# Performance work log

Measured on AMD Instinct MI355X. Metric: run time of the kernel, lower is better.

## Reference

```python
import jax, jax.numpy as jnp
import numpy as np
import math

D_MODEL = 1024
N_HEADS = 8
HEAD_DIM = D_MODEL // N_HEADS
N_CLASSES = 2


def setup_inputs() -> dict:
    key = jax.random.key(0)
    ks = jax.random.split(key, 12)
    s = 1.0 / math.sqrt(D_MODEL)
    return {
        "x": jax.random.normal(ks[0], (8192, D_MODEL), dtype=jnp.float32),
        "class_token": jax.random.normal(ks[1], (1, 1, D_MODEL), dtype=jnp.float32),
        "Wq": jax.random.normal(ks[2], (D_MODEL, D_MODEL), dtype=jnp.float32) * s,
        "bq": jnp.zeros((D_MODEL,), jnp.float32),
        "Wk": jax.random.normal(ks[3], (D_MODEL, D_MODEL), dtype=jnp.float32) * s,
        "bk": jnp.zeros((D_MODEL,), jnp.float32),
        "Wv": jax.random.normal(ks[4], (D_MODEL, D_MODEL), dtype=jnp.float32) * s,
        "bv": jnp.zeros((D_MODEL,), jnp.float32),
        "Wo": jax.random.normal(ks[5], (D_MODEL, D_MODEL), dtype=jnp.float32) * s,
        "bo": jnp.zeros((D_MODEL,), jnp.float32),
        "Wc": jax.random.normal(ks[6], (N_CLASSES, D_MODEL), dtype=jnp.float32) * s,
        "bc": jnp.zeros((N_CLASSES,), jnp.float32),
    }


def reference(x, class_token, Wq, bq, Wk, bk, Wv, bv, Wo, bo, Wc, bc):
    # Prepend class token: [T, D] with T = N_patches + 1 (batch size is 1)
    tokens = jnp.concatenate([class_token.reshape(1, D_MODEL), x], axis=0)
    T = tokens.shape[0]
    scale = 1.0 / math.sqrt(HEAD_DIM)

    def heads(W, b):
        return (tokens @ W.T + b).reshape(T, N_HEADS, HEAD_DIM).transpose(1, 0, 2)

    q = heads(Wq, bq)  # [H, T, hd]
    k = heads(Wk, bk)
    v = heads(Wv, bv)

    scores = jnp.einsum("htd,hsd->hts", q, k) * scale  # [H, T, T]
    probs = jax.nn.softmax(scores, axis=-1)
    attn_out = jnp.einsum("hts,hsd->htd", probs, v)  # [H, T, hd]

    # MIL attention weights: class-token row, over patches, head-averaged
    A = probs[:, 0, 1:].mean(axis=0)[None, :]  # [1, N_patches]

    out = attn_out.transpose(1, 0, 2).reshape(T, D_MODEL) @ Wo.T + bo  # [T, D]
    cls_out = out[0:1]  # [1, D]

    logits = cls_out @ Wc.T + bc  # [1, n_classes]
    y_probs = jax.nn.softmax(logits, axis=1)

    m = jnp.argmax(y_probs.reshape(-1))
    row = m // N_CLASSES
    Y_hat = (m % N_CLASSES)[None]  # [1]
    top_instance = jnp.take(logits, row, axis=0)[None]  # [1, n_classes]
    Y_prob = jnp.take(y_probs, row, axis=0)[None]  # [1, n_classes]

    return top_instance, Y_prob, Y_hat, y_probs, A
```

## Files before the change

kernel.cpp:

```cpp
#include <hip/hip_runtime.h>
#include <math.h>

#define D 1024
#define NH 8
#define T 8193

#define OFF_QCLS  0
#define OFF_EP    1024
#define OFF_W     17408
#define OFF_G     25600
#define OFF_CH    41984
#define OFF_CONST 41992
#define OFF_L     42000
#define OFF_PLOG  44048
#define OFF_SCT   48144

static __device__ __forceinline__ float wred(float v) {
    #pragma unroll
    for (int m = 32; m; m >>= 1) v += __shfl_xor(v, m, 64);
    return v;
}

#define DPPADD(v, ctrl) \
    ((v) + __int_as_float(__builtin_amdgcn_update_dpp( \
        0, __float_as_int(v), (ctrl), 0xf, 0xf, true)))

static __device__ __forceinline__ float wave_total(float v) {
    v = DPPADD(v, 0x111);
    v = DPPADD(v, 0x112);
    v = DPPADD(v, 0x114);
    v = DPPADD(v, 0x118);
    v = DPPADD(v, 0x142);
    v = DPPADD(v, 0x143);
    return __int_as_float(__builtin_amdgcn_readlane(__float_as_int(v), 63));
}

__global__ __launch_bounds__(1024) void k1(const float* __restrict__ Wq,
                                           const float* __restrict__ bq,
                                           const float* __restrict__ ct,
                                           const float* __restrict__ Wc,
                                           const float* __restrict__ Wo,
                                           float* __restrict__ ws) {
    __shared__ float red[16];
    __shared__ float er[4][2][256];
    const int b = blockIdx.x, t = threadIdx.x;
    const int w = t >> 6, lane = t & 63;
    if (b < 256) {
        int grp = t >> 8, f4 = t & 255;
        int r = b * 4 + grp;
        const float4* wr = (const float4*)(Wq + (size_t)r * D);
        const float4* cv = (const float4*)ct;
        float4 a = wr[f4], c = cv[f4];
        float v = a.x*c.x + a.y*c.y + a.z*c.z + a.w*c.w;
        v = wred(v);
        if (lane == 0) red[w] = v;
        __syncthreads();
        if (t < 4)
            ws[OFF_QCLS + b*4 + t] = red[4*t]+red[4*t+1]+red[4*t+2]+red[4*t+3] + bq[b*4 + t];
    } else {
        int idx = b - 256;
        int p = idx >> 2, jq = idx & 3;
        int layer = t >> 8, jl = t & 255;
        int j = jq * 256 + jl;
        int i0 = p * 128 + layer * 32;
        const float* wo = Wo + (size_t)i0 * D + j;
        float a0 = 0.f, a1 = 0.f;
        #pragma unroll 8
        for (int i = 0; i < 32; ++i) {
            float r = wo[(size_t)i * D];
            a0 += Wc[i0 + i] * r;
            a1 += Wc[D + i0 + i] * r;
        }
        er[layer][0][jl] = a0;
        er[layer][1][jl] = a1;
        __syncthreads();
        if (t < 512) {
            int c = t >> 8, jl2 = t & 255;
            ws[OFF_EP + p*2048 + c*1024 + jq*256 + jl2] =
                er[0][c][jl2] + er[1][c][jl2] + er[2][c][jl2] + er[3][c][jl2];
        }
    }
}

__global__ __launch_bounds__(1024) void k2(const float* __restrict__ Wk,
                                           const float* __restrict__ bk,
                                           const float* __restrict__ Wv,
                                           const float* __restrict__ Wc,
                                           const float* __restrict__ bo,
                                           const float* __restrict__ bv,
                                           const float* __restrict__ bc,
                                           float* __restrict__ ws) {
    __shared__ float qh[128];
    __shared__ float el[2][128];
    __shared__ float lw[8][128];
    __shared__ float lg[8][2][128];
    __shared__ float red[32];
    const int b = blockIdx.x, t = threadIdx.x;
    const int w = t >> 6, lane = t & 63;
    if (b < 64) {
        int h = b >> 3, je = b & 7;
        if (t < 128) qh[t] = ws[OFF_QCLS + h*128 + t];
        __syncthreads();
        int layer = t >> 7, jl = t & 127;
        int j = je * 128 + jl, d0 = layer * 16;
        const float* wk = Wk + (size_t)(h*128 + d0) * D + j;
        float acc = 0.f;
        #pragma unroll 8
        for (int d = 0; d < 16; ++d) acc += qh[d0 + d] * wk[(size_t)d * D];
        lw[layer][jl] = acc;
        __syncthreads();
        if (t < 128) {
            float s = 0.f;
            #pragma unroll
            for (int i = 0; i < 8; ++i) s += lw[i][t];
            ws[OFF_W + h*1024 + je*128 + t] = s;
        }
    } else if (b < 128) {
        int hb = b - 64, h = hb >> 3, je = hb & 7;
        if (t < 256) {
            int c = t >> 7, r = t & 127;
            float s = 0.f;
            #pragma unroll
            for (int p = 0; p < 8; ++p) s += ws[OFF_EP + p*2048 + c*1024 + h*128 + r];
            el[c][r] = s;
        }
        __syncthreads();
        int layer = t >> 7, jl = t & 127;
        int j = je * 128 + jl, r0 = layer * 16;
        const float* wv = Wv + (size_t)(h*128 + r0) * D + j;
        float a0 = 0.f, a1 = 0.f;
        #pragma unroll 8
        for (int r = 0; r < 16; ++r) {
            float xv = wv[(size_t)r * D];
            a0 += el[0][r0 + r] * xv;
            a1 += el[1][r0 + r] * xv;
        }
        lg[layer][0][jl] = a0;
        lg[layer][1][jl] = a1;
        __syncthreads();
        if (t < 256) {
            int c = t >> 7, jl2 = t & 127;
            float s = 0.f;
            #pragma unroll
            for (int i = 0; i < 8; ++i) s += lg[i][c][jl2];
            ws[OFF_G + c*8192 + h*1024 + je*128 + jl2] = s;
        }
    } else if (b == 128) {
        int h = t >> 7, d = t & 127;
        float v = ws[OFF_QCLS + h*128 + d] * bk[h*128 + d];
        v = wred(v);
        if (lane == 0) red[w] = v;
        __syncthreads();
        if (t < 8) ws[OFF_CH + t] = red[2*t] + red[2*t+1];
    } else {
        float e0 = 0.f, e1 = 0.f;
        #pragma unroll
        for (int p = 0; p < 8; ++p) {
            e0 += ws[OFF_EP + p*2048 + t];
            e1 += ws[OFF_EP + p*2048 + 1024 + t];
        }
        float v0 = Wc[t]*bo[t] + e0*bv[t];
        float v1 = Wc[D + t]*bo[t] + e1*bv[t];
        v0 = wred(v0); v1 = wred(v1);
        if (lane == 0) { red[w] = v0; red[16 + w] = v1; }
        __syncthreads();
        if (t == 0) {
            float a0 = 0.f, a1 = 0.f;
            #pragma unroll
            for (int i = 0; i < 16; ++i) { a0 += red[i]; a1 += red[16 + i]; }
            ws[OFF_CONST + 0] = a0 + bc[0];
            ws[OFF_CONST + 1] = a1 + bc[1];
        }
    }
}

__global__ __launch_bounds__(512, 2) void k3(const float* __restrict__ x,
                                             const float* __restrict__ ct,
                                             float* __restrict__ ws) {
    __shared__ float stash[33 * D];
    __shared__ float pe[33][8];
    __shared__ float plred[8][8];
    const int b = blockIdx.x, t = threadIdx.x;
    const int w = t >> 6, lane = t & 63;

    float4 wreg[8][4];
    const float4* wg4 = (const float4*)(ws + OFF_W);
    #pragma unroll
    for (int h = 0; h < 8; ++h)
        #pragma unroll
        for (int j = 0; j < 4; ++j)
            wreg[h][j] = wg4[h * 256 + j * 64 + lane];
    float chv[8];
    #pragma unroll
    for (int h = 0; h < 8; ++h) chv[h] = ws[OFF_CH + h];

    const int ntok_blk = (b == 255) ? 33 : 32;
    const bool tail = (b == 255 && w == 7);
    const int ntok_w = tail ? 5 : 4;
    for (int i = 0; i < ntok_w; ++i) {
        int k = (i < 4) ? (w * 4 + i) : 32;
        int s = b * 32 + k;
        const float* row = (s == 0) ? ct : (x + (size_t)(s - 1) * D);
        float* dst = stash + k * D;
        #pragma unroll
        for (int q = 0; q < 4; ++q)
            __builtin_amdgcn_global_load_lds(
                (const __attribute__((address_space(1))) unsigned int*)(row + q * 256 + lane * 4),
                (__attribute__((address_space(3))) unsigned int*)(dst + q * 256),
                16, 0, 0);
    }

    const float scale = 0.08838834764831845f;
    auto compute = [&](int k) {
        int s = b * 32 + k;
        const float4* tk = (const float4*)(stash + k * D);
        float4 t0 = tk[lane], t1 = tk[64 + lane], t2 = tk[128 + lane], t3 = tk[192 + lane];
        float pv[8];
        #pragma unroll
        for (int h = 0; h < 8; ++h) {
            float4 w0 = wreg[h][0], w1 = wreg[h][1], w2 = wreg[h][2], w3 = wreg[h][3];
            float v = w0.x*t0.x + w0.y*t0.y + w0.z*t0.z + w0.w*t0.w
                    + w1.x*t1.x + w1.y*t1.y + w1.z*t1.z + w1.w*t1.w
                    + w2.x*t2.x + w2.y*t2.y + w2.z*t2.z + w2.w*t2.w
                    + w3.x*t3.x + w3.y*t3.y + w3.z*t3.z + w3.w*t3.w;
            v = wave_total(v);
            pv[h] = __expf(scale * (v + chv[h]));
        }
        if (lane == 0) {
            float4* sct = (float4*)(ws + OFF_SCT);
            sct[s * 2]     = make_float4(pv[0], pv[1], pv[2], pv[3]);
            sct[s * 2 + 1] = make_float4(pv[4], pv[5], pv[6], pv[7]);
            *(float4*)&pe[k][0] = make_float4(pv[0], pv[1], pv[2], pv[3]);
            *(float4*)&pe[k][4] = make_float4(pv[4], pv[5], pv[6], pv[7]);
        }
    };

    if (!tail) {
        __builtin_amdgcn_s_waitcnt(0x0f7c); compute(w*4 + 0);
        __builtin_amdgcn_s_waitcnt(0x0f78); compute(w*4 + 1);
        __builtin_amdgcn_s_waitcnt(0x0f74); compute(w*4 + 2);
        __builtin_amdgcn_s_waitcnt(0x0f70); compute(w*4 + 3);
    } else {
        __builtin_amdgcn_s_waitcnt(0x0f70);
        for (int i = 0; i < 5; ++i) compute((i < 4) ? (w*4 + i) : 32);
    }
    __syncthreads();

    if (t < 8) {
        float s = 0.f;
        for (int k = 0; k < ntok_blk; ++k) s += pe[k][t];
        ws[OFF_L + b * 8 + t] = s;
    }

    const int f4 = t & 255, half = t >> 8;
    const float4* st4 = (const float4*)stash;
    float4 acc0 = {0,0,0,0}, acc1 = {0,0,0,0}, acc2 = {0,0,0,0}, acc3 = {0,0,0,0};
    for (int k = 0; k < ntok_blk; ++k) {
        float4 tv = st4[k * 256 + f4];
        float4 pv = *(const float4*)&pe[k][half * 4];
        acc0.x += pv.x*tv.x; acc0.y += pv.x*tv.y; acc0.z += pv.x*tv.z; acc0.w += pv.x*tv.w;
        acc1.x += pv.y*tv.x; acc1.y += pv.y*tv.y; acc1.z += pv.y*tv.z; acc1.w += pv.y*tv.w;
        acc2.x += pv.z*tv.x; acc2.y += pv.z*tv.y; acc2.z += pv.z*tv.z; acc2.w += pv.z*tv.w;
        acc3.x += pv.w*tv.x; acc3.y += pv.w*tv.y; acc3.z += pv.w*tv.z; acc3.w += pv.w*tv.w;
    }

    const float4* G4 = (const float4*)(ws + OFF_G);
    float pl[8];
    #pragma unroll
    for (int c = 0; c < 2; ++c) {
        float4 g0 = G4[c*2048 + (half*4 + 0)*256 + f4];
        float4 g1 = G4[c*2048 + (half*4 + 1)*256 + f4];
        float4 g2 = G4[c*2048 + (half*4 + 2)*256 + f4];
        float4 g3 = G4[c*2048 + (half*4 + 3)*256 + f4];
        pl[c*4+0] = g0.x*acc0.x + g0.y*acc0.y + g0.z*acc0.z + g0.w*acc0.w;
        pl[c*4+1] = g1.x*acc1.x + g1.y*acc1.y + g1.z*acc1.z + g1.w*acc1.w;
        pl[c*4+2] = g2.x*acc2.x + g2.y*acc2.y + g2.z*acc2.z + g2.w*acc2.w;
        pl[c*4+3] = g3.x*acc3.x + g3.y*acc3.y + g3.z*acc3.z + g3.w*acc3.w;
    }
    #pragma unroll
    for (int v = 0; v < 8; ++v) pl[v] = wave_total(pl[v]);
    if (lane == 0)
        #pragma unroll
        for (int v = 0; v < 8; ++v) plred[w][v] = pl[v];
    __syncthreads();
    if (t < 16) {
        int c = t >> 3, hh = t & 7;
        int wb = (hh < 4) ? 0 : 4, vi = c * 4 + (hh & 3);
        ws[OFF_PLOG + b*16 + t] =
            plred[wb][vi] + plred[wb+1][vi] + plred[wb+2][vi] + plred[wb+3][vi];
    }
}

__global__ __launch_bounds__(256) void k4(float* __restrict__ out,
                                          float* __restrict__ ws) {
    __shared__ float lp[32][8];
    __shared__ float rlh[8];
    __shared__ float r2[8];
    const int b = blockIdx.x, t = threadIdx.x;

    {
        int seg = t >> 3, h = t & 7;
        float s = 0.f;
        for (int pb = seg; pb < 256; pb += 32) s += ws[OFF_L + pb*8 + h];
        lp[seg][h] = s;
    }
    __syncthreads();
    if (t < 8) {
        float s = 0.f;
        #pragma unroll
        for (int i = 0; i < 32; ++i) s += lp[i][t];
        rlh[t] = 1.f / s;
    }
    __syncthreads();

    if (t < 32) {
        int s_ = b * 32 + t + 1;
        const float4* sct = (const float4*)(ws + OFF_SCT);
        float4 pa = sct[s_ * 2], pb4 = sct[s_ * 2 + 1];
        float sum = pa.x*rlh[0] + pa.y*rlh[1] + pa.z*rlh[2] + pa.w*rlh[3]
                  + pb4.x*rlh[4] + pb4.y*rlh[5] + pb4.z*rlh[6] + pb4.w*rlh[7];
        out[6 + s_] = sum * 0.125f;
    }

    if (b == 0) {
        float v0 = 0.f, v1 = 0.f;
        for (int idx = t; idx < 4096; idx += 256) {
            float val = ws[OFF_PLOG + idx];
            int rem = idx & 15;
            float z = val * rlh[rem & 7];
            if ((rem >> 3) == 0) v0 += z; else v1 += z;
        }
        v0 = wred(v0); v1 = wred(v1);
        if ((t & 63) == 0) { r2[t >> 6] = v0; r2[4 + (t >> 6)] = v1; }
        __syncthreads();
        if (t == 0) {
            float l0 = r2[0]+r2[1]+r2[2]+r2[3] + ws[OFF_CONST + 0];
            float l1 = r2[4]+r2[5]+r2[6]+r2[7] + ws[OFF_CONST + 1];
            float mx = fmaxf(l0, l1);
            float e0 = __expf(l0 - mx), e1 = __expf(l1 - mx);
            float inv = 1.f / (e0 + e1);
            float p0 = e0 * inv, p1 = e1 * inv;
            int am = (p1 > p0) ? 1 : 0;
            out[0] = l0; out[1] = l1;
            out[2] = p0; out[3] = p1;
            out[4] = (float)am;
            out[5] = p0; out[6] = p1;
        }
    }
}

extern "C" void kernel_launch(void* const* d_in, const int* in_sizes, int n_in,
                              void* d_out, int out_size, void* d_ws, size_t ws_size,
                              hipStream_t stream) {
    const float* x  = (const float*)d_in[0];
    const float* ct = (const float*)d_in[1];
    const float* Wq = (const float*)d_in[2];
    const float* bq = (const float*)d_in[3];
    const float* Wk = (const float*)d_in[4];
    const float* bk = (const float*)d_in[5];
    const float* Wv = (const float*)d_in[6];
    const float* bv = (const float*)d_in[7];
    const float* Wo = (const float*)d_in[8];
    const float* bo = (const float*)d_in[9];
    const float* Wc = (const float*)d_in[10];
    const float* bc = (const float*)d_in[11];
    float* out = (float*)d_out;
    float* ws  = (float*)d_ws;

    k1<<<dim3(288), dim3(1024), 0, stream>>>(Wq, bq, ct, Wc, Wo, ws);
    k2<<<dim3(130), dim3(1024), 0, stream>>>(Wk, bk, Wv, Wc, bo, bv, bc, ws);
    k3<<<dim3(256), dim3(512),  0, stream>>>(x, ct, ws);
    k4<<<dim3(256), dim3(256),  0, stream>>>(out, ws);
}
```

Measured before the change: 123.8 us.

## Fuse final normalization kernel into k3 via last-block atomic counter

Removes the separate k4 launch by having k3 blocks increment an atomic done counter; the last block to finish performs the softmax-denominator reduction, writes the head-averaged attention weights for all 8192 patches, and computes logits and probabilities. The counter is reset in k2. This saves one kernel launch and its gap, but the tail work (8192 outputs) now runs in a single block instead of being spread over 256 blocks, which lengthens the serial tail.

Result: slower. 126.6 us (+2.3%).

```diff
diff --git a/kernel.cpp b/kernel.cpp
--- a/kernel.cpp
+++ b/kernel.cpp
@@ -11,6 +11,7 @@
 #define OFF_G     25600
 #define OFF_CH    41984
 #define OFF_CONST 41992
+#define OFF_DONE  41994
 #define OFF_L     42000
 #define OFF_PLOG  44048
 #define OFF_SCT   48144
@@ -153,6 +154,7 @@
         __syncthreads();
         if (t < 8) ws[OFF_CH + t] = red[2*t] + red[2*t+1];
     } else {
+        if (t == 0) *((unsigned int*)(ws + OFF_DONE)) = 0u;
         float e0 = 0.f, e1 = 0.f;
         #pragma unroll
         for (int p = 0; p < 8; ++p) {
@@ -176,10 +178,15 @@
 
 __global__ __launch_bounds__(512, 2) void k3(const float* __restrict__ x,
                                              const float* __restrict__ ct,
+                                             float* __restrict__ out,
                                              float* __restrict__ ws) {
     __shared__ float stash[33 * D];
     __shared__ float pe[33][8];
     __shared__ float plred[8][8];
+    __shared__ unsigned lastFlag;
+    __shared__ float lp[32][8];
+    __shared__ float rlhs[8];
+    __shared__ float r2a[8], r2b[8];
     const int b = blockIdx.x, t = threadIdx.x;
     const int w = t >> 6, lane = t & 63;
 
@@ -289,16 +296,19 @@
         ws[OFF_PLOG + b*16 + t] =
             plred[wb][vi] + plred[wb+1][vi] + plred[wb+2][vi] + plred[wb+3][vi];
     }
-}
-
-__global__ __launch_bounds__(256) void k4(float* __restrict__ out,
-                                          float* __restrict__ ws) {
-    __shared__ float lp[32][8];
-    __shared__ float rlh[8];
-    __shared__ float r2[8];
-    const int b = blockIdx.x, t = threadIdx.x;
-
-    {
+
+    __syncthreads();
+    if (t == 0) {
+        __threadfence();
+        unsigned old = atomicAdd((unsigned*)(ws + OFF_DONE), 1u);
+        lastFlag = (old == 255) ? 1u : 0u;
+    }
+    __syncthreads();
+    if (!lastFlag) return;
+    if (t == 0) __threadfence();
+    __syncthreads();
+
+    if (t < 256) {
         int seg = t >> 3, h = t & 7;
         float s = 0.f;
         for (int pb = seg; pb < 256; pb += 32) s += ws[OFF_L + pb*8 + h];
@@ -309,33 +319,39 @@
         float s = 0.f;
         #pragma unroll
         for (int i = 0; i < 32; ++i) s += lp[i][t];
-        rlh[t] = 1.f / s;
-    }
-    __syncthreads();
-
-    if (t < 32) {
-        int s_ = b * 32 + t + 1;
-        const float4* sct = (const float4*)(ws + OFF_SCT);
-        float4 pa = sct[s_ * 2], pb4 = sct[s_ * 2 + 1];
-        float sum = pa.x*rlh[0] + pa.y*rlh[1] + pa.z*rlh[2] + pa.w*rlh[3]
-                  + pb4.x*rlh[4] + pb4.y*rlh[5] + pb4.z*rlh[6] + pb4.w*rlh[7];
-        out[6 + s_] = sum * 0.125f;
-    }
-
-    if (b == 0) {
+        rlhs[t] = 1.f / s;
+    }
+    __syncthreads();
+    float rl[8];
+    #pragma unroll
+    for (int h = 0; h < 8; ++h) rl[h] = rlhs[h];
+
+    const float4* sct4 = (const float4*)(ws + OFF_SCT);
+    for (int i = t; i < 8192; i += 512) {
+        int s_ = i + 1;
+        float4 pa = sct4[s_ * 2], pb4 = sct4[s_ * 2 + 1];
+        float sum = pa.x*rl[0] + pa.y*rl[1] + pa.z*rl[2] + pa.w*rl[3]
+                  + pb4.x*rl[4] + pb4.y*rl[5] + pb4.z*rl[6] + pb4.w*rl[7];
+        out[7 + i] = sum * 0.125f;
+    }
+
+    {
         float v0 = 0.f, v1 = 0.f;
-        for (int idx = t; idx < 4096; idx += 256) {
+        for (int idx = t; idx < 4096; idx += 512) {
             float val = ws[OFF_PLOG + idx];
             int rem = idx & 15;
-            float z = val * rlh[rem & 7];
+            float z = val * rl[rem & 7];
             if ((rem >> 3) == 0) v0 += z; else v1 += z;
         }
         v0 = wred(v0); v1 = wred(v1);
-        if ((t & 63) == 0) { r2[t >> 6] = v0; r2[4 + (t >> 6)] = v1; }
+        if (lane == 0) { r2a[w] = v0; r2b[w] = v1; }
         __syncthreads();
         if (t == 0) {
-            float l0 = r2[0]+r2[1]+r2[2]+r2[3] + ws[OFF_CONST + 0];
-            float l1 = r2[4]+r2[5]+r2[6]+r2[7] + ws[OFF_CONST + 1];
+            float a0 = 0.f, a1 = 0.f;
+            #pragma unroll
+            for (int i = 0; i < 8; ++i) { a0 += r2a[i]; a1 += r2b[i]; }
+            float l0 = a0 + ws[OFF_CONST + 0];
+            float l1 = a1 + ws[OFF_CONST + 1];
             float mx = fmaxf(l0, l1);
             float e0 = __expf(l0 - mx), e1 = __expf(l1 - mx);
             float inv = 1.f / (e0 + e1);
@@ -369,6 +385,5 @@
 
     k1<<<dim3(288), dim3(1024), 0, stream>>>(Wq, bq, ct, Wc, Wo, ws);
     k2<<<dim3(130), dim3(1024), 0, stream>>>(Wk, bk, Wv, Wc, bo, bv, bc, ws);
-    k3<<<dim3(256), dim3(512),  0, stream>>>(x, ct, ws);
-    k4<<<dim3(256), dim3(256),  0, stream>>>(out, ws);
-}
+    k3<<<dim3(256), dim3(512),  0, stream>>>(x, ct, out, ws);
+}
```
